# Kernel optimization log

Hardware: AMD Instinct MI355X
Metric: run time of the kernel (lower is better)

The kernel has to match this reference:

```python
import jax, jax.numpy as jnp
import numpy as np

NUM_HEAD = 16
D_MODEL = 1024
D_HEAD = D_MODEL // NUM_HEAD
BATCH = 4
SEQ = 2048


def setup_inputs() -> dict:
    key = jax.random.key(0)
    kq, kk, kv, kw, kb = jax.random.split(key, 5)
    Q = jax.random.normal(kq, (BATCH, SEQ, D_MODEL), dtype=jnp.float32)
    K = jax.random.normal(kk, (BATCH, SEQ, D_MODEL), dtype=jnp.float32)
    V = jax.random.normal(kv, (BATCH, SEQ, D_MODEL), dtype=jnp.float32)
    # nn.Linear weight [out, in] and bias [out]; scaled like torch default init
    Wq_w = jax.random.normal(kw, (D_MODEL, D_MODEL), dtype=jnp.float32) * (1.0 / np.sqrt(D_MODEL))
    Wq_b = jax.random.normal(kb, (D_MODEL,), dtype=jnp.float32) * 0.01
    return {"Q": Q, "K": K, "V": V, "Wq_w": Wq_w, "Wq_b": Wq_b}


def _split_head(x):
    # [b, s, d_model] -> [b, h, s, d_head]
    b, s, _ = x.shape
    return x.reshape(b, s, NUM_HEAD, D_HEAD).transpose(0, 2, 1, 3)


def reference(Q, K, V, Wq_w, Wq_b):
    # NOTE: original module (faithfully) uses Wq for all three projections.
    q = Q @ Wq_w.T + Wq_b
    k = K @ Wq_w.T + Wq_b
    v = V @ Wq_w.T + Wq_b
    q = _split_head(q)  # [b, h, s, dh]
    k = _split_head(k)
    v = _split_head(v)
    scale = 1.0 / jnp.sqrt(jnp.float32(D_HEAD))
    scores = jnp.einsum("bhqd,bhkd->bhqk", q, k) * scale  # [b, h, s, s]
    att_w = jax.nn.softmax(scores, axis=-1)
    out = jnp.einsum("bhqk,bhkd->bhqd", att_w, v)
    out = out.transpose(0, 2, 1, 3).reshape(Q.shape[0], -1, D_MODEL)
    return out, att_w
```

## Files before the change

### kernel.cpp

```cpp
#include <hip/hip_runtime.h>

typedef _Float16 f16;
typedef _Float16 f16x8 __attribute__((ext_vector_type(8)));
typedef _Float16 f16x4 __attribute__((ext_vector_type(4)));
typedef float    f32x4 __attribute__((ext_vector_type(4)));

static constexpr int NBATCH = 4;
static constexpr int NH     = 16;
static constexpr int SQ     = 2048;
static constexpr int DM     = 1024;
static constexpr int DHEAD  = 64;
static constexpr size_t TEL = (size_t)NBATCH * SQ * DM;
static constexpr size_t WEL = (size_t)DM * DM;

static constexpr float QSCALE = 0.125f * 1.4426950408889634f;

#define MFMA32(a, b, c) __builtin_amdgcn_mfma_f32_16x16x32_f16((a), (b), (c), 0, 0, 0)
#define EXP2(x) __builtin_amdgcn_exp2f(x)

#define GLOAD_LDS16(g, l)                                        \
    __builtin_amdgcn_global_load_lds(                            \
        (const __attribute__((address_space(1))) void*)(g),      \
        (__attribute__((address_space(3))) void*)(l), 16, 0, 0)

__global__ __launch_bounds__(256) void cvt_kernel(
    const float* __restrict__ X0, const float* __restrict__ X1,
    const float* __restrict__ X2, const float* __restrict__ W,
    f16* __restrict__ y0, f16* __restrict__ y1,
    f16* __restrict__ y2, f16* __restrict__ yw)
{
    constexpr int CX = (int)(TEL / 8);
    constexpr int CW = (int)(WEL / 8);
    const int total = 3 * CX + CW;
    for (int c = blockIdx.x * blockDim.x + threadIdx.x; c < total;
         c += gridDim.x * blockDim.x) {
        const float* src; f16* dst; int off;
        if (c < CX)            { src = X0; dst = y0; off = c; }
        else if (c < 2 * CX)   { src = X1; dst = y1; off = c - CX; }
        else if (c < 3 * CX)   { src = X2; dst = y2; off = c - 2 * CX; }
        else                   { src = W;  dst = yw; off = c - 3 * CX; }
        const float* p = src + (size_t)off * 8;
        float4 lo = *(const float4*)p;
        float4 hi = *(const float4*)(p + 4);
        f16x8 v;
        v[0] = (f16)lo.x; v[1] = (f16)lo.y; v[2] = (f16)lo.z; v[3] = (f16)lo.w;
        v[4] = (f16)hi.x; v[5] = (f16)hi.y; v[6] = (f16)hi.z; v[7] = (f16)hi.w;
        *(f16x8*)(dst + (size_t)off * 8) = v;
    }
}

template <bool QK>
__global__ __launch_bounds__(256, 2) void proj_kernel(
    const f16* __restrict__ X0, const f16* __restrict__ X1,
    const f16* __restrict__ W, const float* __restrict__ bias,
    f16* __restrict__ d0, f16* __restrict__ d1)
{
    alignas(16) __shared__ f16 la[2][128 * 32];
    alignas(16) __shared__ f16 lb[2][128 * 32];

    const int bid   = blockIdx.x;
    const int which = QK ? (bid >> 9) : 0;
    const int t0    = bid & 511;
    const int nb    = t0 >> 6;
    const int mb    = t0 & 63;
    const f16* __restrict__ X  = (QK && which) ? X1 : X0;
    const f16* __restrict__ A0 = X + (size_t)mb * 128 * DM;
    const f16* __restrict__ B0 = W + (size_t)nb * 128 * DM;

    const int tid  = threadIdx.x;
    const int wave = tid >> 6;
    const int lane = tid & 63;
    const int wr   = wave >> 1, wc = wave & 1;
    const int l16  = lane & 15, g = lane >> 4;
    const int m_base = mb * 128 + wr * 64;
    const int n_base = nb * 128 + wc * 64;

    auto stage = [&](int buf, int k0) {
        #pragma unroll
        for (int half = 0; half < 2; ++half) {
            const int idx = half * 256 + wave * 64 + lane;
            const int row = idx >> 2;
            const int sc  = (idx & 3) ^ ((row >> 1) & 3);
            const int db  = (half * 256 + wave * 64) * 8;
            GLOAD_LDS16(A0 + (size_t)row * DM + k0 + sc * 8, &la[buf][db]);
            GLOAD_LDS16(B0 + (size_t)row * DM + k0 + sc * 8, &lb[buf][db]);
        }
    };

    f32x4 acc[4][4];
    #pragma unroll
    for (int i = 0; i < 4; ++i)
        #pragma unroll
        for (int j = 0; j < 4; ++j)
            acc[i][j] = (f32x4){0.f, 0.f, 0.f, 0.f};

    stage(0, 0);
    __syncthreads();
    for (int t = 0; t < 32; ++t) {
        const int buf = t & 1;
        if (t < 31) stage(buf ^ 1, (t + 1) * 32);
        f16x8 af[4], bf[4];
        #pragma unroll
        for (int qs = 0; qs < 4; ++qs) {
            const int row = wr * 64 + qs * 16 + l16;
            af[qs] = *(const f16x8*)&la[buf][row * 32 +
                                             ((g ^ ((row >> 1) & 3)) << 3)];
        }
        #pragma unroll
        for (int ns = 0; ns < 4; ++ns) {
            const int row = wc * 64 + ns * 16 + l16;
            bf[ns] = *(const f16x8*)&lb[buf][row * 32 +
                                             ((g ^ ((row >> 1) & 3)) << 3)];
        }
        #pragma unroll
        for (int qs = 0; qs < 4; ++qs)
            #pragma unroll
            for (int ns = 0; ns < 4; ++ns)
                acc[qs][ns] = QK ? MFMA32(bf[ns], af[qs], acc[qs][ns])
                                 : MFMA32(af[qs], bf[ns], acc[qs][ns]);
        __syncthreads();
    }

    const int    s_base = m_base & (SQ - 1);
    const int    b      = m_base >> 11;
    const int    h      = nb * 2 + wc;
    const size_t bh     = (size_t)b * NH + h;

    if (QK) {
        f16* __restrict__ dst = which ? d1 : d0;
        const float sc = (which == 0) ? QSCALE : 1.0f;
        #pragma unroll
        for (int qs = 0; qs < 4; ++qs) {
            const int s = s_base + qs * 16 + l16;
            #pragma unroll
            for (int ns = 0; ns < 4; ++ns) {
                float4 bb = *(const float4*)&bias[n_base + ns * 16 + 4 * g];
                f16x4 pk;
                pk[0] = (f16)((acc[qs][ns][0] + bb.x) * sc);
                pk[1] = (f16)((acc[qs][ns][1] + bb.y) * sc);
                pk[2] = (f16)((acc[qs][ns][2] + bb.z) * sc);
                pk[3] = (f16)((acc[qs][ns][3] + bb.w) * sc);
                *(f16x4*)(dst + (bh * SQ + s) * DHEAD + ns * 16 + 4 * g) = pk;
            }
        }
    } else {
        float bv[4];
        #pragma unroll
        for (int ns = 0; ns < 4; ++ns) bv[ns] = bias[n_base + ns * 16 + l16];
        #pragma unroll
        for (int qs = 0; qs < 4; ++qs)
            #pragma unroll
            for (int ns = 0; ns < 4; ++ns) {
                f16x4 pk;
                #pragma unroll
                for (int r = 0; r < 4; ++r) pk[r] = (f16)(acc[qs][ns][r] + bv[ns]);
                const int dh = ns * 16 + l16;
                const int s0 = s_base + qs * 16 + 4 * g;
                *(f16x4*)(d0 + (bh * DHEAD + dh) * SQ + s0) = pk;
            }
    }
}

__global__ __launch_bounds__(256, 4) void attn_kernel(
    const f16* __restrict__ wq, const f16* __restrict__ wk,
    const f16* __restrict__ wv,
    float* __restrict__ out, float* __restrict__ att)
{
    alignas(16) __shared__ f16 lk[2][64 * 64];
    alignas(16) __shared__ f16 lv[2][64 * 64];

    const int tid  = threadIdx.x;
    const int wave = tid >> 6;
    const int lane = tid & 63;
    const int l16  = lane & 15, g = lane >> 4;

    const int bid     = blockIdx.x;
    const int logical = (bid & 7) * 128 + (bid >> 3);
    const int bh      = logical >> 4;
    const int q0      = (logical & 15) * 128 + wave * 32;

    const f16* __restrict__ qp = wq + (size_t)bh * SQ * DHEAD;
    const f16* __restrict__ kp = wk + (size_t)bh * SQ * DHEAD;
    const f16* __restrict__ vp = wv + (size_t)bh * DHEAD * SQ;
    float* __restrict__ attp = att + ((size_t)bh * SQ + q0) * SQ;
    const int b = bh >> 4, h = bh & 15;
    float* __restrict__ outp = out + ((size_t)b * SQ + q0) * DM + h * DHEAD;

    auto stage64 = [&](f16* dst0, const f16* gbase, int stride) {
        #pragma unroll
        for (int half = 0; half < 2; ++half) {
            const int idx = half * 256 + wave * 64 + lane;
            const int row = idx >> 3;
            const int sc  = (idx & 7) ^ (row & 7);
            GLOAD_LDS16(gbase + (size_t)row * stride + sc * 8,
                        dst0 + (size_t)(half * 256 + wave * 64) * 8);
        }
    };
    auto ldk8 = [&](int buf, int row, int c) -> f16x8 {
        return *(const f16x8*)&lk[buf][row * 64 + ((c ^ (row & 7)) << 3)];
    };
    auto ldv4 = [&](int buf, int row, int c_lin, int half8) -> f16x4 {
        return *(const f16x4*)&lv[buf][row * 64 + ((c_lin ^ (row & 7)) << 3) +
                                       half8 * 4];
    };

    f16x8 qf[2][2];
    #pragma unroll
    for (int qs = 0; qs < 2; ++qs)
        #pragma unroll
        for (int dhf = 0; dhf < 2; ++dhf)
            qf[qs][dhf] = *(const f16x8*)(qp + (size_t)(q0 + qs * 16 + l16) * DHEAD +
                                          dhf * 32 + g * 8);

    const f32x4 zero = (f32x4){0.f, 0.f, 0.f, 0.f};
    constexpr int NT = SQ / 64;

    float accl[2] = {0.f, 0.f};
    f32x4 oacc[2][4];
    #pragma unroll
    for (int qs = 0; qs < 2; ++qs)
        #pragma unroll
        for (int ds = 0; ds < 4; ++ds) oacc[qs][ds] = zero;

    stage64(&lk[0][0], kp, DHEAD);
    stage64(&lv[0][0], vp, SQ);
    for (int t = 0; t < NT; ++t) {
        const int buf = t & 1;
        asm volatile("s_waitcnt vmcnt(0)" ::: "memory");
        __builtin_amdgcn_s_barrier();
        if (t + 1 < NT) {
            stage64(&lk[buf ^ 1][0], kp + (size_t)(t + 1) * 64 * DHEAD, DHEAD);
            stage64(&lv[buf ^ 1][0], vp + (t + 1) * 64, SQ);
        }
        #pragma unroll
        for (int p = 0; p < 2; ++p) {
            f16x8 pb8[2];
            #pragma unroll
            for (int hh = 0; hh < 2; ++hh) {
                const int row = p * 32 + hh * 16 + l16;
                f16x8 kf0 = ldk8(buf, row, g);
                f16x8 kf1 = ldk8(buf, row, 4 + g);
                #pragma unroll
                for (int qs = 0; qs < 2; ++qs) {
                    f32x4 sc = MFMA32(kf0, qf[qs][0], zero);
                    sc = MFMA32(kf1, qf[qs][1], sc);
                    float e0 = EXP2(sc[0]), e1 = EXP2(sc[1]);
                    float e2 = EXP2(sc[2]), e3 = EXP2(sc[3]);
                    accl[qs] += (e0 + e1) + (e2 + e3);
                    pb8[qs][hh * 4 + 0] = (f16)e0;
                    pb8[qs][hh * 4 + 1] = (f16)e1;
                    pb8[qs][hh * 4 + 2] = (f16)e2;
                    pb8[qs][hh * 4 + 3] = (f16)e3;
                }
            }
            #pragma unroll
            for (int ds = 0; ds < 4; ++ds) {
                const int vrow = ds * 16 + l16;
                f16x4 va = ldv4(buf, vrow, p * 4 + (g >> 1), g & 1);
                f16x4 vb = ldv4(buf, vrow, p * 4 + 2 + (g >> 1), g & 1);
                f16x8 vf8;
                vf8[0] = va[0]; vf8[1] = va[1]; vf8[2] = va[2]; vf8[3] = va[3];
                vf8[4] = vb[0]; vf8[5] = vb[1]; vf8[6] = vb[2]; vf8[7] = vb[3];
                oacc[0][ds] = MFMA32(vf8, pb8[0], oacc[0][ds]);
                oacc[1][ds] = MFMA32(vf8, pb8[1], oacc[1][ds]);
            }
        }
    }

    float linv[2];
    #pragma unroll
    for (int qs = 0; qs < 2; ++qs) {
        float v = accl[qs];
        v += __shfl_xor(v, 16, 64);
        v += __shfl_xor(v, 32, 64);
        linv[qs] = 1.f / v;
    }

    #pragma unroll
    for (int qs = 0; qs < 2; ++qs)
        #pragma unroll
        for (int ds = 0; ds < 4; ++ds) {
            float4 o;
            o.x = oacc[qs][ds][0] * linv[qs];
            o.y = oacc[qs][ds][1] * linv[qs];
            o.z = oacc[qs][ds][2] * linv[qs];
            o.w = oacc[qs][ds][3] * linv[qs];
            *(float4*)(outp + (size_t)(qs * 16 + l16) * DM + ds * 16 + 4 * g) = o;
        }

    stage64(&lk[0][0], kp, DHEAD);
    __syncthreads();
    for (int t = 0; t < NT; ++t) {
        const int buf = t & 1;
        const int kv0 = t * 64;
        if (t + 1 < NT)
            stage64(&lk[buf ^ 1][0], kp + (size_t)(t + 1) * 64 * DHEAD, DHEAD);
        #pragma unroll
        for (int s16 = 0; s16 < 4; ++s16) {
            const int row = s16 * 16 + l16;
            f16x8 kf0 = ldk8(buf, row, g);
            f16x8 kf1 = ldk8(buf, row, 4 + g);
            #pragma unroll
            for (int qs = 0; qs < 2; ++qs) {
                f32x4 sc = MFMA32(kf0, qf[qs][0], zero);
                sc = MFMA32(kf1, qf[qs][1], sc);
                float4 a;
                a.x = EXP2(sc[0]) * linv[qs];
                a.y = EXP2(sc[1]) * linv[qs];
                a.z = EXP2(sc[2]) * linv[qs];
                a.w = EXP2(sc[3]) * linv[qs];
                *(float4*)(attp + (size_t)(qs * 16 + l16) * SQ + kv0 +
                           s16 * 16 + 4 * g) = a;
            }
        }
        __syncthreads();
    }
}

extern "C" void kernel_launch(void* const* d_in, const int* in_sizes, int n_in,
                              void* d_out, int out_size, void* d_ws, size_t ws_size,
                              hipStream_t stream) {
    const float* Q    = (const float*)d_in[0];
    const float* K    = (const float*)d_in[1];
    const float* V    = (const float*)d_in[2];
    const float* W    = (const float*)d_in[3];
    const float* bias = (const float*)d_in[4];

    f16* wq = (f16*)d_ws;
    f16* wk = wq + TEL;
    f16* wv = wk + TEL;

    float* out = (float*)d_out;
    float* att = out + TEL;

    f16* x0 = (f16*)att;
    f16* x1 = x0 + TEL;
    f16* x2 = x1 + TEL;
    f16* xw = x2 + TEL;

    cvt_kernel <<<2048, 256, 0, stream>>>(Q, K, V, W, x0, x1, x2, xw);
    proj_kernel<true ><<<1024, 256, 0, stream>>>(x0, x1, xw, bias, wq, wk);
    proj_kernel<false><<< 512, 256, 0, stream>>>(x2, nullptr, xw, bias, wv, nullptr);
    attn_kernel<<<1024, 256, 0, stream>>>(wq, wk, wv, out, att);
}
```

Measured before the change: 435.6 us.

## Stagger two query groups so attention writes overlap the PV pass

Each wave now handles two 16-row query groups, A and B, one after the other instead of 32 rows at once. Group A's second pass, which writes the normalized attention weights, is fused into group B's softmax/PV pass. Group B's attention writes then run in a final K-only pass. The aim is to interleave the large fp32 attention-matrix stores with MFMA compute instead of running them as a separate store-bound phase. In exchange, each 16-row group gets half the MFMA work per K/V tile and there are three K sweeps rather than two.

```diff
diff --git a/kernel.cpp b/kernel.cpp
--- a/kernel.cpp
+++ b/kernel.cpp
@@ -177,14 +177,18 @@
     const int bid     = blockIdx.x;
     const int logical = (bid & 7) * 128 + (bid >> 3);
     const int bh      = logical >> 4;
-    const int q0      = (logical & 15) * 128 + wave * 32;
+    const int q0      = (logical & 15) * 128;
 
     const f16* __restrict__ qp = wq + (size_t)bh * SQ * DHEAD;
     const f16* __restrict__ kp = wk + (size_t)bh * SQ * DHEAD;
     const f16* __restrict__ vp = wv + (size_t)bh * DHEAD * SQ;
-    float* __restrict__ attp = att + ((size_t)bh * SQ + q0) * SQ;
+    const int rA = wave * 16;
+    const int rB = 64 + wave * 16;
+    float* __restrict__ attpA = att + ((size_t)bh * SQ + q0 + rA) * SQ;
+    float* __restrict__ attpB = att + ((size_t)bh * SQ + q0 + rB) * SQ;
     const int b = bh >> 4, h = bh & 15;
-    float* __restrict__ outp = out + ((size_t)b * SQ + q0) * DM + h * DHEAD;
+    float* __restrict__ outpA = out + ((size_t)b * SQ + q0 + rA) * DM + h * DHEAD;
+    float* __restrict__ outpB = out + ((size_t)b * SQ + q0 + rB) * DM + h * DHEAD;
 
     auto stage64 = [&](f16* dst0, const f16* gbase, int stride) {
         #pragma unroll
@@ -204,26 +208,79 @@
                                        half8 * 4];
     };
 
-    f16x8 qf[2][2];
-    #pragma unroll
-    for (int qs = 0; qs < 2; ++qs)
-        #pragma unroll
-        for (int dhf = 0; dhf < 2; ++dhf)
-            qf[qs][dhf] = *(const f16x8*)(qp + (size_t)(q0 + qs * 16 + l16) * DHEAD +
-                                          dhf * 32 + g * 8);
+    f16x8 qfA[2], qfB[2];
+    #pragma unroll
+    for (int dhf = 0; dhf < 2; ++dhf) {
+        qfA[dhf] = *(const f16x8*)(qp + (size_t)(q0 + rA + l16) * DHEAD +
+                                   dhf * 32 + g * 8);
+        qfB[dhf] = *(const f16x8*)(qp + (size_t)(q0 + rB + l16) * DHEAD +
+                                   dhf * 32 + g * 8);
+    }
 
     const f32x4 zero = (f32x4){0.f, 0.f, 0.f, 0.f};
     constexpr int NT = SQ / 64;
 
-    float accl[2] = {0.f, 0.f};
-    f32x4 oacc[2][4];
-    #pragma unroll
-    for (int qs = 0; qs < 2; ++qs)
-        #pragma unroll
-        for (int ds = 0; ds < 4; ++ds) oacc[qs][ds] = zero;
+    float accl = 0.f;
+    f32x4 oacc[4];
+    #pragma unroll
+    for (int ds = 0; ds < 4; ++ds) oacc[ds] = zero;
 
     stage64(&lk[0][0], kp, DHEAD);
     stage64(&lv[0][0], vp, SQ);
+    for (int t = 0; t < NT; ++t) {
+        const int buf = t & 1;
+        asm volatile("s_waitcnt vmcnt(0)" ::: "memory");
+        __builtin_amdgcn_s_barrier();
+        {
+            const int nt2 = (t + 1) & (NT - 1);
+            stage64(&lk[buf ^ 1][0], kp + (size_t)nt2 * 64 * DHEAD, DHEAD);
+            stage64(&lv[buf ^ 1][0], vp + nt2 * 64, SQ);
+        }
+        #pragma unroll
+        for (int p = 0; p < 2; ++p) {
+            f16x8 pb8;
+            #pragma unroll
+            for (int hh = 0; hh < 2; ++hh) {
+                const int row = p * 32 + hh * 16 + l16;
+                f16x8 kf0 = ldk8(buf, row, g);
+                f16x8 kf1 = ldk8(buf, row, 4 + g);
+                f32x4 sc = MFMA32(kf0, qfA[0], zero);
+                sc = MFMA32(kf1, qfA[1], sc);
+                float e0 = EXP2(sc[0]), e1 = EXP2(sc[1]);
+                float e2 = EXP2(sc[2]), e3 = EXP2(sc[3]);
+                accl += (e0 + e1) + (e2 + e3);
+                pb8[hh * 4 + 0] = (f16)e0; pb8[hh * 4 + 1] = (f16)e1;
+                pb8[hh * 4 + 2] = (f16)e2; pb8[hh * 4 + 3] = (f16)e3;
+            }
+            #pragma unroll
+            for (int ds = 0; ds < 4; ++ds) {
+                const int vrow = ds * 16 + l16;
+                f16x4 va = ldv4(buf, vrow, p * 4 + (g >> 1), g & 1);
+                f16x4 vb = ldv4(buf, vrow, p * 4 + 2 + (g >> 1), g & 1);
+                f16x8 vf8;
+                vf8[0] = va[0]; vf8[1] = va[1]; vf8[2] = va[2]; vf8[3] = va[3];
+                vf8[4] = vb[0]; vf8[5] = vb[1]; vf8[6] = vb[2]; vf8[7] = vb[3];
+                oacc[ds] = MFMA32(vf8, pb8, oacc[ds]);
+            }
+        }
+    }
+    float linvA;
+    {
+        float v = accl;
+        v += __shfl_xor(v, 16, 64);
+        v += __shfl_xor(v, 32, 64);
+        linvA = 1.f / v;
+    }
+    #pragma unroll
+    for (int ds = 0; ds < 4; ++ds) {
+        float4 o;
+        o.x = oacc[ds][0] * linvA; o.y = oacc[ds][1] * linvA;
+        o.z = oacc[ds][2] * linvA; o.w = oacc[ds][3] * linvA;
+        *(float4*)(outpA + (size_t)l16 * DM + ds * 16 + 4 * g) = o;
+        oacc[ds] = zero;
+    }
+    accl = 0.f;
+
     for (int t = 0; t < NT; ++t) {
         const int buf = t & 1;
         asm volatile("s_waitcnt vmcnt(0)" ::: "memory");
@@ -231,27 +288,31 @@
         if (t + 1 < NT) {
             stage64(&lk[buf ^ 1][0], kp + (size_t)(t + 1) * 64 * DHEAD, DHEAD);
             stage64(&lv[buf ^ 1][0], vp + (t + 1) * 64, SQ);
+        } else {
+            stage64(&lk[buf ^ 1][0], kp, DHEAD);
         }
         #pragma unroll
         for (int p = 0; p < 2; ++p) {
-            f16x8 pb8[2];
+            f16x8 pb8;
             #pragma unroll
             for (int hh = 0; hh < 2; ++hh) {
                 const int row = p * 32 + hh * 16 + l16;
                 f16x8 kf0 = ldk8(buf, row, g);
                 f16x8 kf1 = ldk8(buf, row, 4 + g);
-                #pragma unroll
-                for (int qs = 0; qs < 2; ++qs) {
-                    f32x4 sc = MFMA32(kf0, qf[qs][0], zero);
-                    sc = MFMA32(kf1, qf[qs][1], sc);
-                    float e0 = EXP2(sc[0]), e1 = EXP2(sc[1]);
-                    float e2 = EXP2(sc[2]), e3 = EXP2(sc[3]);
-                    accl[qs] += (e0 + e1) + (e2 + e3);
-                    pb8[qs][hh * 4 + 0] = (f16)e0;
-                    pb8[qs][hh * 4 + 1] = (f16)e1;
-                    pb8[qs][hh * 4 + 2] = (f16)e2;
-                    pb8[qs][hh * 4 + 3] = (f16)e3;
-                }
+                f32x4 sA = MFMA32(kf0, qfA[0], zero);
+                sA = MFMA32(kf1, qfA[1], sA);
+                float4 a;
+                a.x = EXP2(sA[0]) * linvA; a.y = EXP2(sA[1]) * linvA;
+                a.z = EXP2(sA[2]) * linvA; a.w = EXP2(sA[3]) * linvA;
+                *(float4*)(attpA + (size_t)l16 * SQ + t * 64 + p * 32 +
+                           hh * 16 + 4 * g) = a;
+                f32x4 sB = MFMA32(kf0, qfB[0], zero);
+                sB = MFMA32(kf1, qfB[1], sB);
+                float e0 = EXP2(sB[0]), e1 = EXP2(sB[1]);
+                float e2 = EXP2(sB[2]), e3 = EXP2(sB[3]);
+                accl += (e0 + e1) + (e2 + e3);
+                pb8[hh * 4 + 0] = (f16)e0; pb8[hh * 4 + 1] = (f16)e1;
+                pb8[hh * 4 + 2] = (f16)e2; pb8[hh * 4 + 3] = (f16)e3;
             }
             #pragma unroll
             for (int ds = 0; ds < 4; ++ds) {
@@ -261,38 +322,29 @@
                 f16x8 vf8;
                 vf8[0] = va[0]; vf8[1] = va[1]; vf8[2] = va[2]; vf8[3] = va[3];
                 vf8[4] = vb[0]; vf8[5] = vb[1]; vf8[6] = vb[2]; vf8[7] = vb[3];
-                oacc[0][ds] = MFMA32(vf8, pb8[0], oacc[0][ds]);
-                oacc[1][ds] = MFMA32(vf8, pb8[1], oacc[1][ds]);
-            }
-        }
-    }
-
-    float linv[2];
-    #pragma unroll
-    for (int qs = 0; qs < 2; ++qs) {
-        float v = accl[qs];
+                oacc[ds] = MFMA32(vf8, pb8, oacc[ds]);
+            }
+        }
+    }
+    float linvB;
+    {
+        float v = accl;
         v += __shfl_xor(v, 16, 64);
         v += __shfl_xor(v, 32, 64);
-        linv[qs] = 1.f / v;
-    }
-
-    #pragma unroll
-    for (int qs = 0; qs < 2; ++qs)
-        #pragma unroll
-        for (int ds = 0; ds < 4; ++ds) {
-            float4 o;
-            o.x = oacc[qs][ds][0] * linv[qs];
-            o.y = oacc[qs][ds][1] * linv[qs];
-            o.z = oacc[qs][ds][2] * linv[qs];
-            o.w = oacc[qs][ds][3] * linv[qs];
-            *(float4*)(outp + (size_t)(qs * 16 + l16) * DM + ds * 16 + 4 * g) = o;
-        }
-
-    stage64(&lk[0][0], kp, DHEAD);
-    __syncthreads();
+        linvB = 1.f / v;
+    }
+    #pragma unroll
+    for (int ds = 0; ds < 4; ++ds) {
+        float4 o;
+        o.x = oacc[ds][0] * linvB; o.y = oacc[ds][1] * linvB;
+        o.z = oacc[ds][2] * linvB; o.w = oacc[ds][3] * linvB;
+        *(float4*)(outpB + (size_t)l16 * DM + ds * 16 + 4 * g) = o;
+    }
+
     for (int t = 0; t < NT; ++t) {
         const int buf = t & 1;
-        const int kv0 = t * 64;
+        asm volatile("s_waitcnt vmcnt(0)" ::: "memory");
+        __builtin_amdgcn_s_barrier();
         if (t + 1 < NT)
             stage64(&lk[buf ^ 1][0], kp + (size_t)(t + 1) * 64 * DHEAD, DHEAD);
         #pragma unroll
@@ -300,20 +352,13 @@
             const int row = s16 * 16 + l16;
             f16x8 kf0 = ldk8(buf, row, g);
             f16x8 kf1 = ldk8(buf, row, 4 + g);
-            #pragma unroll
-            for (int qs = 0; qs < 2; ++qs) {
-                f32x4 sc = MFMA32(kf0, qf[qs][0], zero);
-                sc = MFMA32(kf1, qf[qs][1], sc);
-                float4 a;
-                a.x = EXP2(sc[0]) * linv[qs];
-                a.y = EXP2(sc[1]) * linv[qs];
-                a.z = EXP2(sc[2]) * linv[qs];
-                a.w = EXP2(sc[3]) * linv[qs];
-                *(float4*)(attp + (size_t)(qs * 16 + l16) * SQ + kv0 +
-                           s16 * 16 + 4 * g) = a;
-            }
-        }
-        __syncthreads();
+            f32x4 sB = MFMA32(kf0, qfB[0], zero);
+            sB = MFMA32(kf1, qfB[1], sB);
+            float4 a;
+            a.x = EXP2(sB[0]) * linvB; a.y = EXP2(sB[1]) * linvB;
+            a.z = EXP2(sB[2]) * linvB; a.w = EXP2(sB[3]) * linvB;
+            *(float4*)(attpB + (size_t)l16 * SQ + t * 64 + s16 * 16 + 4 * g) = a;
+        }
     }
 }
 
```

New measurement: 500.7 us. +14.9%, slower.

## Merge loop barriers and use nontemporal stores for attention and output writes

Applied to the files above, without the earlier changes.

In the projection GEMM, the two __syncthreads per iteration become a single s_waitcnt plus s_barrier at the top of the loop. In the attention-weight pass, the end-of-tile barrier waits with vmcnt(8), so the preceding global stores can stay in flight while the next K tile's LDS load must still complete. The large att and out writes switch to nontemporal stores to avoid polluting the cache. The hand-tuned vmcnt depends on how many stores the compiler emits per tile; if that count is wrong, the wait can return before the LDS loads land and the kernel reads stale data.

```diff
diff --git a/kernel.cpp b/kernel.cpp
--- a/kernel.cpp
+++ b/kernel.cpp
@@ -95,9 +95,10 @@
             acc[i][j] = (f32x4){0.f, 0.f, 0.f, 0.f};
 
     stage(0, 0);
-    __syncthreads();
     for (int t = 0; t < 32; ++t) {
         const int buf = t & 1;
+        asm volatile("s_waitcnt vmcnt(0)" ::: "memory");
+        __builtin_amdgcn_s_barrier();
         if (t < 31) stage(buf ^ 1, (t + 1) * 32);
         f16x8 af[4], bf[4];
         #pragma unroll
@@ -118,7 +119,6 @@
             for (int ns = 0; ns < 4; ++ns)
                 acc[qs][ns] = QK ? MFMA32(bf[ns], af[qs], acc[qs][ns])
                                  : MFMA32(af[qs], bf[ns], acc[qs][ns]);
-        __syncthreads();
     }
 
     const int    s_base = m_base & (SQ - 1);
@@ -280,16 +280,18 @@
     for (int qs = 0; qs < 2; ++qs)
         #pragma unroll
         for (int ds = 0; ds < 4; ++ds) {
-            float4 o;
-            o.x = oacc[qs][ds][0] * linv[qs];
-            o.y = oacc[qs][ds][1] * linv[qs];
-            o.z = oacc[qs][ds][2] * linv[qs];
-            o.w = oacc[qs][ds][3] * linv[qs];
-            *(float4*)(outp + (size_t)(qs * 16 + l16) * DM + ds * 16 + 4 * g) = o;
+            f32x4 o;
+            o[0] = oacc[qs][ds][0] * linv[qs];
+            o[1] = oacc[qs][ds][1] * linv[qs];
+            o[2] = oacc[qs][ds][2] * linv[qs];
+            o[3] = oacc[qs][ds][3] * linv[qs];
+            __builtin_nontemporal_store(
+                o, (f32x4*)(outp + (size_t)(qs * 16 + l16) * DM + ds * 16 + 4 * g));
         }
 
     stage64(&lk[0][0], kp, DHEAD);
-    __syncthreads();
+    asm volatile("s_waitcnt vmcnt(0)" ::: "memory");
+    __builtin_amdgcn_s_barrier();
     for (int t = 0; t < NT; ++t) {
         const int buf = t & 1;
         const int kv0 = t * 64;
@@ -304,16 +306,20 @@
             for (int qs = 0; qs < 2; ++qs) {
                 f32x4 sc = MFMA32(kf0, qf[qs][0], zero);
                 sc = MFMA32(kf1, qf[qs][1], sc);
-                float4 a;
-                a.x = EXP2(sc[0]) * linv[qs];
-                a.y = EXP2(sc[1]) * linv[qs];
-                a.z = EXP2(sc[2]) * linv[qs];
-                a.w = EXP2(sc[3]) * linv[qs];
-                *(float4*)(attp + (size_t)(qs * 16 + l16) * SQ + kv0 +
-                           s16 * 16 + 4 * g) = a;
-            }
-        }
-        __syncthreads();
+                f32x4 a;
+                a[0] = EXP2(sc[0]) * linv[qs];
+                a[1] = EXP2(sc[1]) * linv[qs];
+                a[2] = EXP2(sc[2]) * linv[qs];
+                a[3] = EXP2(sc[3]) * linv[qs];
+                __builtin_nontemporal_store(
+                    a, (f32x4*)(attp + (size_t)(qs * 16 + l16) * SQ + kv0 +
+                                s16 * 16 + 4 * g));
+            }
+        }
+        if (t + 1 < NT) {
+            asm volatile("s_waitcnt vmcnt(8)" ::: "memory");
+            __builtin_amdgcn_s_barrier();
+        }
     }
 }
 
```

Measured after the change: 500.5 us. 1.15x slower.
